# Kernel tuning notes

Hardware: AMD Instinct MI355X
Metric: run time of the kernel (lower is better)

## Reference

```python
import jax, jax.numpy as jnp
import numpy as np

NUM_HEADS = 12

def _attn(q, k, v, scale):
    # q,k,v: [..., L, hd]; softmax attention over L (key axis)
    s = jnp.einsum('...qd,...kd->...qk', q, k) * scale
    a = jax.nn.softmax(s, axis=-1)
    return jnp.einsum('...qk,...kd->...qd', a, v)

def setup_inputs() -> dict:
    key = jax.random.key(0)
    k1, k2, k3 = jax.random.split(key, 3)
    B, N, C, D = 8, 256, 16, 768
    x = jax.random.normal(k1, (B, N, C, D), dtype=jnp.float32)
    w_qkv = jax.random.normal(k2, (D, 6 * D), dtype=jnp.float32) * (D ** -0.5)
    w_proj = jax.random.normal(k3, (D, D), dtype=jnp.float32) * (D ** -0.5)
    b_proj = jnp.zeros((D,), dtype=jnp.float32)
    return {"x": x, "w_qkv": w_qkv, "w_proj": w_proj, "b_proj": b_proj}

def reference(x, w_qkv, w_proj, b_proj):
    B, N, C, D = x.shape
    H = NUM_HEADS
    hd = D // H
    scale = hd ** -0.5
    # qkv: [B,N,C,6,H,hd] -> [6,B,H,N,C,hd]
    qkv = (x @ w_qkv).reshape(B, N, C, 6, H, hd).transpose(3, 0, 4, 1, 2, 5)
    qc, kc, qs, ks, vc, vs = qkv[0], qkv[1], qkv[2], qkv[3], qkv[4], qkv[5]
    # spatial attention over N (per channel c): move to [B,H,C,N,hd]
    qs = jnp.swapaxes(qs, -2, -3)
    ks = jnp.swapaxes(ks, -2, -3)
    vs = jnp.swapaxes(vs, -2, -3)
    xs = _attn(qs, ks, vs, scale)          # [B,H,C,N,hd]
    xs = jnp.swapaxes(xs, -2, -3)          # [B,H,N,C,hd]
    # channel attention over C (per token n)
    xc = _attn(qc, kc, vc, scale)          # [B,H,N,C,hd]
    out = xs * xc                           # elementwise combine (fused path)
    # matches torch: x.transpose(1,2).reshape(B,N,C,D)
    out = out.transpose(0, 2, 1, 3, 4).reshape(B, N, C, D)
    return out @ w_proj + b_proj
```

## Files before the change

### kernel.cpp

```cpp
#include <hip/hip_runtime.h>

typedef _Float16 f16;
typedef f16  f16x8 __attribute__((ext_vector_type(8)));
typedef float f32x4 __attribute__((ext_vector_type(4)));

#define S3 3145728LL

__device__ __forceinline__ f32x4 mm(f16x8 a, f16x8 b, f32x4 c) {
  return __builtin_amdgcn_mfma_f32_16x16x32_f16(a, b, c, 0, 0, 0);
}
__device__ __forceinline__ void BAR() { asm volatile("s_barrier" ::: "memory"); }

__device__ __forceinline__ int esw(int t, int col) {
  return t * 128 + ((((col >> 3) ^ ((t ^ (t >> 3)) & 7)) << 3) | (col & 7));
}
__device__ __forceinline__ int oesw(int t, int col) {
  return t * 64 + ((((col >> 3) ^ (t & 7)) << 3) | (col & 7));
}

__global__ void cvt_T_kernel(const float* __restrict__ in, f16* __restrict__ out,
                             int R, int Cc) {
  __shared__ float tile[32][33];
  int tc = blockIdx.x, tr = blockIdx.y;
  int lr = threadIdx.x & 31, lw = threadIdx.x >> 5;
  int c0 = tc * 32, r0 = tr * 32;
#pragma unroll
  for (int i = 0; i < 4; i++)
    tile[lw + 8 * i][lr] = in[(size_t)(r0 + lw + 8 * i) * Cc + c0 + lr];
  __syncthreads();
#pragma unroll
  for (int i = 0; i < 4; i++)
    out[(size_t)(c0 + lw + 8 * i) * R + r0 + lr] = (f16)tile[lr][lw + 8 * i];
}

__global__ void cvt_x_kernel(const float* __restrict__ in, f16* __restrict__ out) {
  size_t i = ((size_t)blockIdx.x * 256 + threadIdx.x) * 8;
  f32x4 a = __builtin_nontemporal_load((const f32x4*)(in + i));
  f32x4 b = __builtin_nontemporal_load((const f32x4*)(in + i + 4));
  f16x8 o;
#pragma unroll
  for (int j = 0; j < 4; j++) { o[j] = (f16)a[j]; o[4 + j] = (f16)b[j]; }
  *(f16x8*)(out + i) = o;
}

#define QST_A(c, q, kt) __builtin_amdgcn_global_load_lds( \
    (const __attribute__((address_space(1))) void*)(aSrc + (size_t)(q) * 24576 + (size_t)(kt) * 64), \
    (__attribute__((address_space(3))) void*)((char*)lds + (c) * 32768 + (q) * 1024 * 4 + wave * 1024), 16, 0, 0)
#define QST_B(c, q, kt) __builtin_amdgcn_global_load_lds( \
    (const __attribute__((address_space(1))) void*)(bSrc + (size_t)(q) * 24576 + (size_t)(kt) * 64), \
    (__attribute__((address_space(3))) void*)((char*)lds + 16384 + (c) * 32768 + (q) * 1024 * 4 + wave * 1024), 16, 0, 0)

__global__ __launch_bounds__(256, 2) void gemm_qkvT(
    const f16* __restrict__ A, const f16* __restrict__ Bt,
    f16* __restrict__ area, long long cstr_) {
  __shared__ f16 lds[32768];
  size_t cstr = (size_t)cstr_;
  int id  = blockIdx.x;
  int cpx = gridDim.x >> 3;
  int id2 = (id & 7) * cpx + (id >> 3);
  int sr = id2 / 288, rr = id2 % 288;
  int bm = sr * 8 + (rr & 7), bn = rr >> 3;

  int tid = threadIdx.x;
  int wave = tid >> 6, lane = tid & 63;
  int l16 = lane & 15, lq = lane >> 4;
  int wr = wave >> 1, wc = wave & 1;
  int l7 = l16 & 7;
  int cb0 = ((lq) ^ l7) << 4;
  int cb1 = ((4 + lq) ^ l7) << 4;

  const f16* aSrc = A  + (size_t)(bm * 128 + (tid >> 3)) * 768 +
                    (((tid & 7) ^ ((tid >> 3) & 7)) << 3);
  const f16* bSrc = Bt + (size_t)(bn * 128 + (tid >> 3)) * 768 +
                    (((tid & 7) ^ ((tid >> 3) & 7)) << 3);

  f32x4 zz = {0.f, 0.f, 0.f, 0.f};
  f32x4 acc[4][4];
#pragma unroll
  for (int m = 0; m < 4; m++)
#pragma unroll
    for (int n = 0; n < 4; n++) acc[m][n] = zz;

#pragma unroll
  for (int q = 0; q < 4; q++) { QST_A(0, q, 0); }
#pragma unroll
  for (int q = 0; q < 4; q++) { QST_B(0, q, 0); }
#pragma unroll
  for (int q = 0; q < 4; q++) { QST_A(1, q, 1); }
#pragma unroll
  for (int q = 0; q < 4; q++) { QST_B(1, q, 1); }
  asm volatile("s_waitcnt vmcnt(8)" ::: "memory");
  BAR();

  f16x8 af[4][2], bf[4][2];
#pragma unroll 2
  for (int t = 0; t < 12; ++t) {
    int c = t & 1;
    const char* ab = (const char*)lds + c * 32768;
    const char* bb = ab + 16384;
    int rA = wr * 64 + l16;
    int rB = wc * 64 + l16;
#pragma unroll
    for (int mf = 0; mf < 4; mf++) {
      af[mf][0] = *(const f16x8*)(ab + (rA + mf * 16) * 128 + cb0);
      af[mf][1] = *(const f16x8*)(ab + (rA + mf * 16) * 128 + cb1);
    }
#pragma unroll
    for (int nf = 0; nf < 4; nf++) {
      bf[nf][0] = *(const f16x8*)(bb + (rB + nf * 16) * 128 + cb0);
      bf[nf][1] = *(const f16x8*)(bb + (rB + nf * 16) * 128 + cb1);
    }
    asm volatile("s_waitcnt lgkmcnt(0)" ::: "memory");
    BAR();
    if (t < 10) {
#pragma unroll
      for (int q = 0; q < 4; q++) { QST_A(c, q, t + 2); }
#pragma unroll
      for (int q = 0; q < 4; q++) { QST_B(c, q, t + 2); }
    }
    __builtin_amdgcn_s_setprio(1);
#pragma unroll
    for (int ks = 0; ks < 2; ks++)
#pragma unroll
      for (int mf = 0; mf < 4; mf++)
#pragma unroll
        for (int nf = 0; nf < 4; nf++)
          acc[mf][nf] = mm(af[mf][ks], bf[nf][ks], acc[mf][nf]);
    __builtin_amdgcn_s_setprio(0);
    if (t < 10) asm volatile("s_waitcnt vmcnt(8)" ::: "memory");
    else        asm volatile("s_waitcnt vmcnt(0)" ::: "memory");
    BAR();
  }

  int s  = bn / 6;
  int h0 = (bn % 6) * 2;
  size_t comp;
  if (s == 0) comp = 0; else if (s == 1) comp = 1; else if (s == 2) comp = 3;
  else if (s == 3) comp = 4; else if (s == 4) comp = 2; else comp = 5;
  int g = (bm * 128) >> 12;
  size_t base = comp * cstr + (size_t)g * S3;
  int n0 = (bm & 31) * 8;

  __syncthreads();
#pragma unroll
  for (int mi = 0; mi < 4; mi++)
#pragma unroll
    for (int ni = 0; ni < 4; ni++)
#pragma unroll
      for (int r = 0; r < 4; r++) {
        int t = wr * 64 + mi * 16 + lq * 4 + r;
        int col = wc * 64 + ni * 16 + l16;
        lds[esw(t, col)] = (f16)acc[mi][ni][r];
      }
  __syncthreads();

  if (s < 2) {
#pragma unroll
    for (int i = 0; i < 4; i++) {
      int u = wave * 4 + i;
      int hl = u >> 3, j16 = u & 7;
#pragma unroll
      for (int half = 0; half < 2; half++) {
        int e0 = half * 512 + lane * 8;
        int cc = e0 >> 6, d0 = e0 & 63;
        f16x8 v = *(const f16x8*)&lds[esw(j16 * 16 + cc, hl * 64 + d0)];
        __builtin_nontemporal_store(v, (f16x8*)&area[base +
            (size_t)(h0 + hl) * 262144 + (size_t)(n0 + j16) * 1024 + e0]);
      }
    }
  } else if (s < 4) {
#pragma unroll
    for (int i = 0; i < 8; i++) {
      int u = wave * 8 + i;
      int hl = u >> 4, cc = u & 15;
      int e = lane * 8;
      int nl = e >> 6, d0 = e & 63;
      f16x8 v = *(const f16x8*)&lds[esw(nl * 16 + cc, hl * 64 + d0)];
      __builtin_nontemporal_store(v, (f16x8*)&area[base +
          (size_t)((h0 + hl) * 16 + cc) * 16384 + (size_t)n0 * 64 + e]);
    }
  } else if (s == 4) {
#pragma unroll
    for (int i = 0; i < 4; i++) {
      int u = wave * 4 + i;
      int hl = u >> 3, j8 = u & 7;
#pragma unroll
      for (int half = 0; half < 2; half++) {
        int e0 = half * 512 + lane * 8;
        int d0 = e0 >> 4, cb = e0 & 15;
        f16x8 v;
#pragma unroll
        for (int j = 0; j < 8; j++)
          v[j] = lds[esw(j8 * 16 + cb + j, hl * 64 + d0)];
        __builtin_nontemporal_store(v, (f16x8*)&area[base +
            (size_t)((h0 + hl) * 256 + n0 + j8) * 1024 + e0]);
      }
    }
  } else {
#pragma unroll
    for (int i = 0; i < 8; i++) {
      int u = wave * 8 + i;
      int hl = u >> 4, cc = u & 15;
      int e = lane * 8;
      int d0 = e >> 3;
      f16x8 v;
#pragma unroll
      for (int j = 0; j < 8; j++)
        v[j] = lds[esw(j * 16 + cc, hl * 64 + d0)];
      __builtin_nontemporal_store(v, (f16x8*)&area[base +
          ((size_t)((h0 + hl) * 16 + cc) * 32 + (bm & 31)) * 512 + e]);
    }
  }
}

#define STG_A(c, q, kt) __builtin_amdgcn_global_load_lds( \
    (const __attribute__((address_space(1))) void*)(aSrc + (size_t)(q) * 49152 + (size_t)(kt) * 64), \
    (__attribute__((address_space(3))) void*)(lds + (c) * 32768 + (q) * 4096 + wave * 512), 16, 0, 0)
#define STG_B(c, q, kt) __builtin_amdgcn_global_load_lds( \
    (const __attribute__((address_space(1))) void*)(bSrc + (size_t)(q) * 49152 + (size_t)(kt) * 64), \
    (__attribute__((address_space(3))) void*)(lds + 16384 + (c) * 32768 + (q) * 4096 + wave * 512), 16, 0, 0)

__global__ __launch_bounds__(512, 2) void gemm_proj8(
    const f16* __restrict__ A, const f16* __restrict__ Bt,
    const float* __restrict__ bias, float* __restrict__ Cout) {
  __shared__ f16 lds[65536];
  int id  = blockIdx.x;
  int cpx = gridDim.x >> 3;
  int id2 = (id & 7) * cpx + (id >> 3);
  int sr = id2 / 24, rr = id2 % 24;
  int bm = sr * 8 + (rr & 7), bn = rr >> 3;

  int tid = threadIdx.x;
  int wave = tid >> 6, lane = tid & 63;
  int l16 = lane & 15, lq = lane >> 4;
  int wr = wave >> 2, wc = wave & 3;
  int sx  = (l16 & 7) << 4;
  int cb0 = (lq * 16) ^ sx;
  int cb1 = (64 + lq * 16) ^ sx;

  int scol = ((tid & 7) ^ ((tid >> 3) & 7)) << 3;
  const f16* aSrc = A  + (size_t)(bm * 256 + (tid >> 3)) * 768 + scol;
  const f16* bSrc = Bt + (size_t)(bn * 256 + (tid >> 3)) * 768 + scol;

  f32x4 zz = {0.f, 0.f, 0.f, 0.f};
  f32x4 acc[8][4];
#pragma unroll
  for (int m = 0; m < 8; m++)
#pragma unroll
    for (int n = 0; n < 4; n++) acc[m][n] = zz;

  STG_A(0, 0, 0); STG_A(0, 1, 0); STG_A(0, 2, 0); STG_A(0, 3, 0);
  STG_B(0, 0, 0); STG_B(0, 1, 0); STG_B(0, 2, 0); STG_B(0, 3, 0);
  STG_A(1, 1, 1); STG_A(1, 3, 1);
  STG_B(1, 0, 1); STG_B(1, 1, 1);
  asm volatile("s_waitcnt vmcnt(4)" ::: "memory");
  BAR();

  f16x8 af[4][2], ag[4][2], bf[2][2], bg[2][2];
#pragma unroll 2
  for (int t = 0; t < 12; ++t) {
    int c = t & 1, nb = c ^ 1;
    const char* ab = (const char*)lds + c * 65536;
    const char* bb = ab + 32768;
    int rA = wr * 128 + l16;
    int rB = wc * 64 + l16;
#pragma unroll
    for (int mf = 0; mf < 4; mf++) {
      af[mf][0] = *(const f16x8*)(ab + (rA + mf * 16) * 128 + cb0);
      af[mf][1] = *(const f16x8*)(ab + (rA + mf * 16) * 128 + cb1);
    }
#pragma unroll
    for (int nf = 0; nf < 2; nf++) {
      bf[nf][0] = *(const f16x8*)(bb + (rB + nf * 16) * 128 + cb0);
      bf[nf][1] = *(const f16x8*)(bb + (rB + nf * 16) * 128 + cb1);
      bg[nf][0] = *(const f16x8*)(bb + (rB + 32 + nf * 16) * 128 + cb0);
      bg[nf][1] = *(const f16x8*)(bb + (rB + 32 + nf * 16) * 128 + cb1);
    }
    if (t < 11) {
      STG_B(nb, 2, t + 1); STG_B(nb, 3, t + 1);
      STG_A(nb, 0, t + 1); STG_A(nb, 2, t + 1);
    }
    BAR();
    __builtin_amdgcn_s_setprio(1);
#pragma unroll
    for (int ks = 0; ks < 2; ks++)
#pragma unroll
      for (int mf = 0; mf < 4; mf++)
#pragma unroll
        for (int nf = 0; nf < 2; nf++) {
          acc[mf][nf]     = mm(af[mf][ks], bf[nf][ks], acc[mf][nf]);
          acc[mf][2 + nf] = mm(af[mf][ks], bg[nf][ks], acc[mf][2 + nf]);
        }
    __builtin_amdgcn_s_setprio(0);
    BAR();
#pragma unroll
    for (int mf = 0; mf < 4; mf++) {
      ag[mf][0] = *(const f16x8*)(ab + (rA + 64 + mf * 16) * 128 + cb0);
      ag[mf][1] = *(const f16x8*)(ab + (rA + 64 + mf * 16) * 128 + cb1);
    }
    if (t < 10) {
      STG_A(c, 1, t + 2); STG_A(c, 3, t + 2);
      STG_B(c, 0, t + 2); STG_B(c, 1, t + 2);
    }
    BAR();
    __builtin_amdgcn_s_setprio(1);
#pragma unroll
    for (int ks = 0; ks < 2; ks++)
#pragma unroll
      for (int mf = 0; mf < 4; mf++)
#pragma unroll
        for (int nf = 0; nf < 2; nf++) {
          acc[4 + mf][nf]     = mm(ag[mf][ks], bf[nf][ks], acc[4 + mf][nf]);
          acc[4 + mf][2 + nf] = mm(ag[mf][ks], bg[nf][ks], acc[4 + mf][2 + nf]);
        }
    __builtin_amdgcn_s_setprio(0);
    if (t < 10) asm volatile("s_waitcnt vmcnt(4)" ::: "memory");
    else        asm volatile("s_waitcnt vmcnt(0)" ::: "memory");
    BAR();
  }

#pragma unroll
  for (int ni = 0; ni < 4; ni++) {
    int col = bn * 256 + wc * 64 + ni * 16 + l16;
    float bb = bias[col];
#pragma unroll
    for (int mi = 0; mi < 8; mi++) {
#pragma unroll
      for (int r = 0; r < 4; r++) {
        int row = bm * 256 + wr * 128 + (mi >> 2) * 64 + (mi & 3) * 16 + lq * 4 + r;
        __builtin_nontemporal_store(acc[mi][ni][r] + bb,
                                    &Cout[(size_t)row * 768 + col]);
      }
    }
  }
}

__global__ __launch_bounds__(512) void attn_spat_kernel(f16* __restrict__ area,
                                                        long long cstr_) {
  size_t cstr = (size_t)cstr_;
  int blk = blockIdx.x;
  int g = blk / 192, rem = blk % 192;
  int h = rem >> 4, c = rem & 15;
  size_t goff = (size_t)g * S3;
  const f16* qs = area + 3 * cstr + goff + (size_t)((h * 16 + c) * 256) * 64;
  const f16* ks = area + 4 * cstr + goff + (size_t)((h * 16 + c) * 256) * 64;
  const f16* vsb = area + 5 * cstr + goff + (size_t)(h * 16 + c) * 16384;
  f16* xsn = area + 6 * cstr + goff;

  int tid = threadIdx.x;
  int wave = tid >> 6, lane = tid & 63;
  int l16 = lane & 15, lq = lane >> 4;
  __shared__ f16 plds[8][32][40];
  __shared__ f16 osm[16384];

  f32x4 zz = {0.f, 0.f, 0.f, 0.f};
  f16x8 aq[2][2];
#pragma unroll
  for (int m = 0; m < 2; m++)
#pragma unroll
    for (int kd = 0; kd < 2; kd++)
      aq[m][kd] = *(const f16x8*)&qs[(size_t)(wave * 32 + m * 16 + l16) * 64 + kd * 32 + lq * 8];

  f32x4 o[2][4];
  float mrow[2][4], lrow[2][4];
#pragma unroll
  for (int m = 0; m < 2; m++) {
#pragma unroll
    for (int n = 0; n < 4; n++) o[m][n] = zz;
#pragma unroll
    for (int r = 0; r < 4; r++) { mrow[m][r] = -1e30f; lrow[m][r] = 0.f; }
  }

  for (int kc = 0; kc < 8; kc++) {
    int k0 = kc * 32;
    f16x8 bk00 = *(const f16x8*)&ks[(size_t)(k0 + l16) * 64 + lq * 8];
    f16x8 bk01 = *(const f16x8*)&ks[(size_t)(k0 + l16) * 64 + 32 + lq * 8];
    f16x8 bk10 = *(const f16x8*)&ks[(size_t)(k0 + 16 + l16) * 64 + lq * 8];
    f16x8 bk11 = *(const f16x8*)&ks[(size_t)(k0 + 16 + l16) * 64 + 32 + lq * 8];
    f32x4 st[2][2];
#pragma unroll
    for (int m = 0; m < 2; m++) {
      st[m][0] = mm(aq[m][1], bk01, mm(aq[m][0], bk00, zz));
      st[m][1] = mm(aq[m][1], bk11, mm(aq[m][0], bk10, zz));
    }
#pragma unroll
    for (int m = 0; m < 2; m++) {
#pragma unroll
      for (int r = 0; r < 4; r++) {
        float s0 = st[m][0][r] * 0.125f, s1 = st[m][1][r] * 0.125f;
        float t = fmaxf(s0, s1);
        t = fmaxf(t, __shfl_xor(t, 1));
        t = fmaxf(t, __shfl_xor(t, 2));
        t = fmaxf(t, __shfl_xor(t, 4));
        t = fmaxf(t, __shfl_xor(t, 8));
        float mold = mrow[m][r];
        float mnew = fmaxf(mold, t);
        float fac  = __expf(mold - mnew);
        mrow[m][r] = mnew;
        float p0 = __expf(s0 - mnew), p1 = __expf(s1 - mnew);
        lrow[m][r] = lrow[m][r] * fac + p0 + p1;
        o[m][0][r] *= fac; o[m][1][r] *= fac; o[m][2][r] *= fac; o[m][3][r] *= fac;
        int prow = m * 16 + lq * 4 + r;
        plds[wave][prow][l16]      = (f16)p0;
        plds[wave][prow][16 + l16] = (f16)p1;
      }
    }
    f16x8 ap0 = *(const f16x8*)&plds[wave][l16][lq * 8];
    f16x8 ap1 = *(const f16x8*)&plds[wave][16 + l16][lq * 8];
#pragma unroll
    for (int n = 0; n < 4; n++) {
      f16x8 bv = *(const f16x8*)&vsb[((k0 >> 3) + lq) * 512 + (n * 16 + l16) * 8];
      o[0][n] = mm(ap0, bv, o[0][n]);
      o[1][n] = mm(ap1, bv, o[1][n]);
    }
  }
#pragma unroll
  for (int m = 0; m < 2; m++)
#pragma unroll
    for (int r = 0; r < 4; r++) {
      float l = lrow[m][r];
      l += __shfl_xor(l, 1);
      l += __shfl_xor(l, 2);
      l += __shfl_xor(l, 4);
      l += __shfl_xor(l, 8);
      lrow[m][r] = 1.0f / l;
    }
#pragma unroll
  for (int m = 0; m < 2; m++)
#pragma unroll
    for (int n = 0; n < 4; n++)
#pragma unroll
      for (int r = 0; r < 4; r++) {
        int row = wave * 32 + m * 16 + lq * 4 + r;
        osm[oesw(row, n * 16 + l16)] = (f16)(o[m][n][r] * lrow[m][r]);
      }
  __syncthreads();
  size_t hc64 = (size_t)(h * 16 + c) * 64;
#pragma unroll
  for (int i = 0; i < 4; i++) {
    int row = i * 64 + (tid >> 3);
    int dp  = (tid & 7) * 8;
    f16x8 v = *(const f16x8*)&osm[oesw(row, dp)];
    __builtin_nontemporal_store(v, (f16x8*)&xsn[(size_t)row * 12288 + hc64 + dp]);
  }
}

__global__ __launch_bounds__(256) void attn_chan_kernel(f16* __restrict__ area,
                                                        long long cstr_) {
  size_t cstr = (size_t)cstr_;
  int blk = blockIdx.x;
  int g = blk >> 8, n = blk & 255;
  size_t goff = (size_t)g * S3;
  int tid = threadIdx.x;
  int wave = tid >> 6, lane = tid & 63;
  int l16 = lane & 15, lq = lane >> 4;
  __shared__ f16 xsl[12288];
  __shared__ f16 prl[12288];
  __shared__ f16 plds[4][16][40];

  const f16* xsn = area + 6 * cstr + goff + (size_t)n * 12288;
#pragma unroll
  for (int i = 0; i < 6; i++) {
    int seg = wave * 6 + i;
    __builtin_amdgcn_global_load_lds(
        (const __attribute__((address_space(1))) void*)(xsn + seg * 512 + lane * 8),
        (__attribute__((address_space(3))) void*)((char*)xsl + seg * 1024), 16, 0, 0);
  }
  if (lane < 16) {
#pragma unroll
    for (int j = 0; j < 16; j++) plds[wave][lane][16 + j] = (f16)0.f;
  }
  asm volatile("s_waitcnt vmcnt(0)" ::: "memory");
  __syncthreads();

  f32x4 zz = {0.f, 0.f, 0.f, 0.f};
  for (int hi = 0; hi < 3; hi++) {
    int h = wave + hi * 4;
    const f16* q = area + 0 * cstr + goff + (size_t)((h * 256 + n) * 16) * 64;
    const f16* k = area + 1 * cstr + goff + (size_t)((h * 256 + n) * 16) * 64;
    const f16* v = area + 2 * cstr + goff + (size_t)((h * 256 + n) * 64) * 16;
    f16x8 a0 = *(const f16x8*)&q[l16 * 64 + lq * 8];
    f16x8 a1 = *(const f16x8*)&q[l16 * 64 + 32 + lq * 8];
    f16x8 b0 = *(const f16x8*)&k[l16 * 64 + lq * 8];
    f16x8 b1 = *(const f16x8*)&k[l16 * 64 + 32 + lq * 8];
    f32x4 s = mm(a1, b1, mm(a0, b0, zz));
    float p[4];
#pragma unroll
    for (int r = 0; r < 4; r++) {
      float t = s[r] * 0.125f;
      float mx = t;
      mx = fmaxf(mx, __shfl_xor(mx, 1));
      mx = fmaxf(mx, __shfl_xor(mx, 2));
      mx = fmaxf(mx, __shfl_xor(mx, 4));
      mx = fmaxf(mx, __shfl_xor(mx, 8));
      float e = __expf(t - mx);
      float sum = e;
      sum += __shfl_xor(sum, 1);
      sum += __shfl_xor(sum, 2);
      sum += __shfl_xor(sum, 4);
      sum += __shfl_xor(sum, 8);
      p[r] = e / sum;
    }
#pragma unroll
    for (int r = 0; r < 4; r++)
      plds[wave][lq * 4 + r][l16] = (f16)p[r];
    f16x8 ap = *(const f16x8*)&plds[wave][l16][lq * 8];
#pragma unroll
    for (int nt = 0; nt < 4; nt++) {
      f16x8 bv = *(const f16x8*)&v[(nt * 16 + l16) * 16 + lq * 8];
      f32x4 o = mm(ap, bv, zz);
#pragma unroll
      for (int r = 0; r < 4; r++) {
        int cq = lq * 4 + r, d = nt * 16 + l16;
        int idx = h * 1024 + cq * 64 + d;
        float xsv = (float)xsl[idx];
        prl[idx] = (f16)(o[r] * xsv);
      }
    }
  }
  __syncthreads();
  f16* prod = area + 7 * cstr + goff + (size_t)n * 12288;
#pragma unroll
  for (int i = 0; i < 6; i++) {
    f16x8 v = *(const f16x8*)&prl[i * 2048 + tid * 8];
    __builtin_nontemporal_store(v, (f16x8*)&prod[i * 2048 + tid * 8]);
  }
}

extern "C" void kernel_launch(void* const* d_in, const int* in_sizes, int n_in,
                              void* d_out, int out_size, void* d_ws, size_t ws_size,
                              hipStream_t stream) {
  const float* x      = (const float*)d_in[0];
  const float* w_qkv  = (const float*)d_in[1];
  const float* w_proj = (const float*)d_in[2];
  const float* b_proj = (const float*)d_in[3];
  float* out = (float*)d_out;
  f16* ws = (f16*)d_ws;

  const size_t W16T = 4608ull * 768;
  const size_t WPT  = 768ull * 768;
  f16* w16t = ws;
  f16* wpt  = ws + W16T;
  f16* area = wpt + WPT;

  int G = 8;
  while (G > 1 && (W16T + WPT + 8ull * G * S3) * 2 > ws_size) G >>= 1;
  int nch = 8 / G;
  long long cstr = (long long)G * S3;
  f16* x16 = area + 7 * (size_t)cstr;

  cvt_T_kernel<<<dim3(144, 24), 256, 0, stream>>>(w_qkv, w16t, 768, 4608);
  cvt_T_kernel<<<dim3(24, 24), 256, 0, stream>>>(w_proj, wpt, 768, 768);

  for (int ch = 0; ch < nch; ch++) {
    size_t b0 = (size_t)ch * G;
    cvt_x_kernel<<<G * 1536, 256, 0, stream>>>(x + b0 * S3, x16);
    gemm_qkvT<<<G * 1152, 256, 0, stream>>>(x16, w16t, area, cstr);
    attn_spat_kernel<<<G * 192, 512, 0, stream>>>(area, cstr);
    attn_chan_kernel<<<G * 256, 256, 0, stream>>>(area, cstr);
    gemm_proj8<<<G * 48, 512, 0, stream>>>(area + 7 * (size_t)cstr, wpt, b_proj,
                                           out + b0 * S3);
  }
}
```

Baseline: 544.1 us.

## Shrink projection GEMM tile to 128x128 and reuse dead qs buffer

The projection GEMM moves from 256x256 tiles with 512 threads and a split two-phase inner loop to 128x128 tiles with 256 threads. Each iteration now issues both A and B prefetches two k-steps ahead in one phase, giving a simpler pipeline and a grid four times larger for better CU occupancy. The channel-attention product is written into the spatial-query slot, which is dead by then, so the workspace needs seven slabs instead of eight and may fit a larger batch group per chunk. The smaller tiles lower operand reuse and raise global and LDS traffic per FLOP.

```diff
diff --git a/kernel.cpp b/kernel.cpp
--- a/kernel.cpp
+++ b/kernel.cpp
@@ -213,56 +213,55 @@
   }
 }
 
-#define STG_A(c, q, kt) __builtin_amdgcn_global_load_lds( \
-    (const __attribute__((address_space(1))) void*)(aSrc + (size_t)(q) * 49152 + (size_t)(kt) * 64), \
-    (__attribute__((address_space(3))) void*)(lds + (c) * 32768 + (q) * 4096 + wave * 512), 16, 0, 0)
-#define STG_B(c, q, kt) __builtin_amdgcn_global_load_lds( \
-    (const __attribute__((address_space(1))) void*)(bSrc + (size_t)(q) * 49152 + (size_t)(kt) * 64), \
-    (__attribute__((address_space(3))) void*)(lds + 16384 + (c) * 32768 + (q) * 4096 + wave * 512), 16, 0, 0)
-
-__global__ __launch_bounds__(512, 2) void gemm_proj8(
-    const f16* __restrict__ A, const f16* __restrict__ Bt,
+__global__ __launch_bounds__(256, 2) void gemm_projT(
+    const f16* __restrict__ A,
+    const f16* __restrict__ Bt,
     const float* __restrict__ bias, float* __restrict__ Cout) {
-  __shared__ f16 lds[65536];
+  __shared__ f16 lds[32768];
   int id  = blockIdx.x;
   int cpx = gridDim.x >> 3;
   int id2 = (id & 7) * cpx + (id >> 3);
-  int sr = id2 / 24, rr = id2 % 24;
+  int sr = id2 / 48, rr = id2 % 48;
   int bm = sr * 8 + (rr & 7), bn = rr >> 3;
 
   int tid = threadIdx.x;
   int wave = tid >> 6, lane = tid & 63;
   int l16 = lane & 15, lq = lane >> 4;
-  int wr = wave >> 2, wc = wave & 3;
-  int sx  = (l16 & 7) << 4;
-  int cb0 = (lq * 16) ^ sx;
-  int cb1 = (64 + lq * 16) ^ sx;
-
-  int scol = ((tid & 7) ^ ((tid >> 3) & 7)) << 3;
-  const f16* aSrc = A  + (size_t)(bm * 256 + (tid >> 3)) * 768 + scol;
-  const f16* bSrc = Bt + (size_t)(bn * 256 + (tid >> 3)) * 768 + scol;
+  int wr = wave >> 1, wc = wave & 1;
+  int l7 = l16 & 7;
+  int cb0 = ((lq) ^ l7) << 4;
+  int cb1 = ((4 + lq) ^ l7) << 4;
+
+  const f16* aSrc = A  + (size_t)(bm * 128 + (tid >> 3)) * 768 +
+                    (((tid & 7) ^ ((tid >> 3) & 7)) << 3);
+  const f16* bSrc = Bt + (size_t)(bn * 128 + (tid >> 3)) * 768 +
+                    (((tid & 7) ^ ((tid >> 3) & 7)) << 3);
 
   f32x4 zz = {0.f, 0.f, 0.f, 0.f};
-  f32x4 acc[8][4];
-#pragma unroll
-  for (int m = 0; m < 8; m++)
+  f32x4 acc[4][4];
+#pragma unroll
+  for (int m = 0; m < 4; m++)
 #pragma unroll
     for (int n = 0; n < 4; n++) acc[m][n] = zz;
 
-  STG_A(0, 0, 0); STG_A(0, 1, 0); STG_A(0, 2, 0); STG_A(0, 3, 0);
-  STG_B(0, 0, 0); STG_B(0, 1, 0); STG_B(0, 2, 0); STG_B(0, 3, 0);
-  STG_A(1, 1, 1); STG_A(1, 3, 1);
-  STG_B(1, 0, 1); STG_B(1, 1, 1);
-  asm volatile("s_waitcnt vmcnt(4)" ::: "memory");
+#pragma unroll
+  for (int q = 0; q < 4; q++) { QST_A(0, q, 0); }
+#pragma unroll
+  for (int q = 0; q < 4; q++) { QST_B(0, q, 0); }
+#pragma unroll
+  for (int q = 0; q < 4; q++) { QST_A(1, q, 1); }
+#pragma unroll
+  for (int q = 0; q < 4; q++) { QST_B(1, q, 1); }
+  asm volatile("s_waitcnt vmcnt(8)" ::: "memory");
   BAR();
 
-  f16x8 af[4][2], ag[4][2], bf[2][2], bg[2][2];
+  f16x8 af[4][2], bf[4][2];
 #pragma unroll 2
   for (int t = 0; t < 12; ++t) {
-    int c = t & 1, nb = c ^ 1;
-    const char* ab = (const char*)lds + c * 65536;
-    const char* bb = ab + 32768;
-    int rA = wr * 128 + l16;
+    int c = t & 1;
+    const char* ab = (const char*)lds + c * 32768;
+    const char* bb = ab + 16384;
+    int rA = wr * 64 + l16;
     int rB = wc * 64 + l16;
 #pragma unroll
     for (int mf = 0; mf < 4; mf++) {
@@ -270,64 +269,41 @@
       af[mf][1] = *(const f16x8*)(ab + (rA + mf * 16) * 128 + cb1);
     }
 #pragma unroll
-    for (int nf = 0; nf < 2; nf++) {
+    for (int nf = 0; nf < 4; nf++) {
       bf[nf][0] = *(const f16x8*)(bb + (rB + nf * 16) * 128 + cb0);
       bf[nf][1] = *(const f16x8*)(bb + (rB + nf * 16) * 128 + cb1);
-      bg[nf][0] = *(const f16x8*)(bb + (rB + 32 + nf * 16) * 128 + cb0);
-      bg[nf][1] = *(const f16x8*)(bb + (rB + 32 + nf * 16) * 128 + cb1);
-    }
-    if (t < 11) {
-      STG_B(nb, 2, t + 1); STG_B(nb, 3, t + 1);
-      STG_A(nb, 0, t + 1); STG_A(nb, 2, t + 1);
-    }
+    }
+    asm volatile("s_waitcnt lgkmcnt(0)" ::: "memory");
     BAR();
+    if (t < 10) {
+#pragma unroll
+      for (int q = 0; q < 4; q++) { QST_A(c, q, t + 2); }
+#pragma unroll
+      for (int q = 0; q < 4; q++) { QST_B(c, q, t + 2); }
+    }
     __builtin_amdgcn_s_setprio(1);
 #pragma unroll
     for (int ks = 0; ks < 2; ks++)
 #pragma unroll
       for (int mf = 0; mf < 4; mf++)
 #pragma unroll
-        for (int nf = 0; nf < 2; nf++) {
-          acc[mf][nf]     = mm(af[mf][ks], bf[nf][ks], acc[mf][nf]);
-          acc[mf][2 + nf] = mm(af[mf][ks], bg[nf][ks], acc[mf][2 + nf]);
-        }
+        for (int nf = 0; nf < 4; nf++)
+          acc[mf][nf] = mm(af[mf][ks], bf[nf][ks], acc[mf][nf]);
     __builtin_amdgcn_s_setprio(0);
-    BAR();
-#pragma unroll
-    for (int mf = 0; mf < 4; mf++) {
-      ag[mf][0] = *(const f16x8*)(ab + (rA + 64 + mf * 16) * 128 + cb0);
-      ag[mf][1] = *(const f16x8*)(ab + (rA + 64 + mf * 16) * 128 + cb1);
-    }
-    if (t < 10) {
-      STG_A(c, 1, t + 2); STG_A(c, 3, t + 2);
-      STG_B(c, 0, t + 2); STG_B(c, 1, t + 2);
-    }
-    BAR();
-    __builtin_amdgcn_s_setprio(1);
-#pragma unroll
-    for (int ks = 0; ks < 2; ks++)
-#pragma unroll
-      for (int mf = 0; mf < 4; mf++)
-#pragma unroll
-        for (int nf = 0; nf < 2; nf++) {
-          acc[4 + mf][nf]     = mm(ag[mf][ks], bf[nf][ks], acc[4 + mf][nf]);
-          acc[4 + mf][2 + nf] = mm(ag[mf][ks], bg[nf][ks], acc[4 + mf][2 + nf]);
-        }
-    __builtin_amdgcn_s_setprio(0);
-    if (t < 10) asm volatile("s_waitcnt vmcnt(4)" ::: "memory");
+    if (t < 10) asm volatile("s_waitcnt vmcnt(8)" ::: "memory");
     else        asm volatile("s_waitcnt vmcnt(0)" ::: "memory");
     BAR();
   }
 
 #pragma unroll
   for (int ni = 0; ni < 4; ni++) {
-    int col = bn * 256 + wc * 64 + ni * 16 + l16;
+    int col = bn * 128 + wc * 64 + ni * 16 + l16;
     float bb = bias[col];
 #pragma unroll
-    for (int mi = 0; mi < 8; mi++) {
+    for (int mi = 0; mi < 4; mi++) {
 #pragma unroll
       for (int r = 0; r < 4; r++) {
-        int row = bm * 256 + wr * 128 + (mi >> 2) * 64 + (mi & 3) * 16 + lq * 4 + r;
+        int row = bm * 128 + wr * 64 + mi * 16 + lq * 4 + r;
         __builtin_nontemporal_store(acc[mi][ni][r] + bb,
                                     &Cout[(size_t)row * 768 + col]);
       }
@@ -519,7 +495,7 @@
     }
   }
   __syncthreads();
-  f16* prod = area + 7 * cstr + goff + (size_t)n * 12288;
+  f16* prod = area + 3 * cstr + goff + (size_t)n * 12288;
 #pragma unroll
   for (int i = 0; i < 6; i++) {
     f16x8 v = *(const f16x8*)&prl[i * 2048 + tid * 8];
@@ -544,10 +520,10 @@
   f16* area = wpt + WPT;
 
   int G = 8;
-  while (G > 1 && (W16T + WPT + 8ull * G * S3) * 2 > ws_size) G >>= 1;
+  while (G > 1 && (W16T + WPT + 7ull * G * S3) * 2 > ws_size) G >>= 1;
   int nch = 8 / G;
   long long cstr = (long long)G * S3;
-  f16* x16 = area + 7 * (size_t)cstr;
+  f16* x16 = area + 6 * (size_t)cstr;
 
   cvt_T_kernel<<<dim3(144, 24), 256, 0, stream>>>(w_qkv, w16t, 768, 4608);
   cvt_T_kernel<<<dim3(24, 24), 256, 0, stream>>>(w_proj, wpt, 768, 768);
@@ -558,7 +534,7 @@
     gemm_qkvT<<<G * 1152, 256, 0, stream>>>(x16, w16t, area, cstr);
     attn_spat_kernel<<<G * 192, 512, 0, stream>>>(area, cstr);
     attn_chan_kernel<<<G * 256, 256, 0, stream>>>(area, cstr);
-    gemm_proj8<<<G * 48, 512, 0, stream>>>(area + 7 * (size_t)cstr, wpt, b_proj,
-                                           out + b0 * S3);
-  }
-}
+    gemm_projT<<<G * 192, 256, 0, stream>>>(area + 3 * (size_t)cstr, wpt, b_proj,
+                                            out + b0 * S3);
+  }
+}
```

New measurement: 508.2 us. 1.07x faster.
